# Optimization experiments

Hardware: AMD Instinct MI355X
Metric: run time of the kernel (lower is better)

The kernel has to match this reference:

```python
import jax, jax.numpy as jnp
import numpy as np

L, B, S, E, H, V = 2, 64, 64, 1024, 1024, 32000


def _uni(key, shape, k):
    return jax.random.uniform(key, shape, jnp.float32, -k, k)


def setup_inputs() -> dict:
    key = jax.random.key(0)
    ks = jax.random.split(key, 16)
    k = 1.0 / np.sqrt(H)
    inp = {
        "inputs": jax.random.randint(ks[0], (S, B), 0, V),
        "hidden": jnp.zeros((L, B, H), jnp.float32),
        "emb": jax.random.uniform(ks[1], (V, E), jnp.float32, -0.1, 0.1),
        # per-layer GRU weights stacked on leading L axis (layer0 input = emb = H)
        "Wx": _uni(ks[2], (L, H, H), k),   # linear_W (no bias), used for r gate
        "Ur": _uni(ks[3], (L, H, H), k),
        "br": _uni(ks[4], (L, H), k),
        "Wz": _uni(ks[5], (L, H, H), k),
        "Uz": _uni(ks[6], (L, H, H), k),
        "bz": _uni(ks[7], (L, H), k),
        "Wh": _uni(ks[8], (L, H, H), k),
        "Uh": _uni(ks[9], (L, H, H), k),
        "bh": _uni(ks[10], (L, H), k),
        "dec_W": jax.random.uniform(ks[11], (V, H), jnp.float32, -0.1, 0.1),
        "dec_b": jnp.zeros((V,), jnp.float32),
    }
    return inp


def _gru_cell(x, h, Wx, Ur, br, Wz, Uz, bz, Wh, Uh, bh):
    # faithful to GRU_Hidden.forward (r gate uses linear_W, bias-free W projections)
    r = jax.nn.sigmoid(x @ Wx.T + h @ Ur.T + br)
    z = jax.nn.sigmoid(x @ Wz.T + h @ Uz.T + bz)
    h_cand = jnp.tanh(x @ Wh.T + (r * h) @ Uh.T + bh)
    return (1.0 - z) * h + z * h_cand


def reference(inputs, hidden, emb, Wx, Ur, br, Wz, Uz, bz, Wh, Uh, bh, dec_W, dec_b):
    x_embs = emb[inputs]  # [S, B, E]; dropout is identity (dp_keep_prob = 1.0)
    n_layers = Wx.shape[0]

    def step(h, x_t):
        new_h = []
        inp = x_t
        for l in range(n_layers):
            hl = _gru_cell(inp, h[l], Wx[l], Ur[l], br[l], Wz[l], Uz[l], bz[l], Wh[l], Uh[l], bh[l])
            new_h.append(hl)
            inp = hl
        logits_t = inp @ dec_W.T + dec_b  # [B, V]
        return jnp.stack(new_h), logits_t

    h_final, logits = jax.lax.scan(step, hidden, x_embs)
    return logits, h_final
```

## Files before the change

kernel.cpp:

```cpp
#include <hip/hip_runtime.h>

#define SBV 131072000

typedef __bf16 bf16x8 __attribute__((ext_vector_type(8)));
typedef float  f32x4  __attribute__((ext_vector_type(4)));
typedef unsigned short u16;

__device__ __forceinline__ u16 f2bf(float f) {
  union { float f; unsigned u; } c; c.f = f;
  return (u16)((c.u + 0x7fffu + ((c.u >> 16) & 1u)) >> 16);
}
__device__ __forceinline__ float sigm(float x) { return 1.f / (1.f + __expf(-x)); }
__device__ __forceinline__ float tanh_f(float x) { return 2.f / (1.f + __expf(-2.f * x)) - 1.f; }


__global__ void k_cvtv(const float* __restrict__ src, u16* __restrict__ dst, int n4) {
  const float4* s4 = (const float4*)src;
  ushort4* d4 = (ushort4*)dst;
  for (int i = blockIdx.x * blockDim.x + threadIdx.x; i < n4; i += gridDim.x * blockDim.x) {
    float4 v = s4[i];
    ushort4 o; o.x = f2bf(v.x); o.y = f2bf(v.y); o.z = f2bf(v.z); o.w = f2bf(v.w);
    d4[i] = o;
  }
}

__global__ void k_pack3(const float* __restrict__ sx, const float* __restrict__ sz,
                        const float* __restrict__ sh, int srcOff, u16* __restrict__ dst) {
  int i = blockIdx.x * blockDim.x + threadIdx.x;
  if (i >= 786432) return;
  int g = i >> 18;
  int r4 = i & 262143;
  const float* s = (g == 0 ? sx : (g == 1 ? sz : sh)) + srcOff;
  float4 v = ((const float4*)s)[r4];
  ushort4 o; o.x = f2bf(v.x); o.y = f2bf(v.y); o.z = f2bf(v.z); o.w = f2bf(v.w);
  ((ushort4*)dst)[i] = o;
}

__global__ void k_embed(const int* __restrict__ idx, const float* __restrict__ emb,
                        u16* __restrict__ xe) {
  int i = blockIdx.x * blockDim.x + threadIdx.x;
  if (i >= 1048576) return;
  int row = i >> 8, k4 = i & 255;
  int e = idx[row];
  float4 v = ((const float4*)emb)[(size_t)e * 256 + k4];
  ushort4 o; o.x = f2bf(v.x); o.y = f2bf(v.y); o.z = f2bf(v.z); o.w = f2bf(v.w);
  ((ushort4*)xe)[i] = o;
}

__global__ __launch_bounds__(256) void gemm_bt(const u16* __restrict__ A, const u16* __restrict__ Bm,
                                               float* __restrict__ C, int M, int N, int K, int mtiles) {
  __shared__ u16 As[128 * 32];
  __shared__ u16 Bs[128 * 32];
  const int tid = threadIdx.x;
  const int bm = blockIdx.x % mtiles, bn = blockIdx.x / mtiles;
  const int m0 = bm * 128, n0 = bn * 128;
  const int lane = tid & 63, w = tid >> 6, wm = w & 1, wn = w >> 1;
  const int la = lane & 15, lk = lane >> 4;
  const int srow = tid >> 2, sk = (tid & 3) * 8;
  f32x4 acc[4][4] = {};
  for (int kt = 0; kt < K; kt += 32) {
    const u16* srcA0 = A + (size_t)(m0 + srow) * K + kt + sk;
    const u16* srcA1 = A + (size_t)(m0 + srow + 64) * K + kt + sk;
    const u16* srcB0 = Bm + (size_t)(n0 + srow) * K + kt + sk;
    const u16* srcB1 = Bm + (size_t)(n0 + srow + 64) * K + kt + sk;
    __builtin_amdgcn_global_load_lds((const __attribute__((address_space(1))) void*)srcA0,
        (__attribute__((address_space(3))) void*)((char*)As + tid * 16), 16, 0, 0);
    __builtin_amdgcn_global_load_lds((const __attribute__((address_space(1))) void*)srcA1,
        (__attribute__((address_space(3))) void*)((char*)As + 4096 + tid * 16), 16, 0, 0);
    __builtin_amdgcn_global_load_lds((const __attribute__((address_space(1))) void*)srcB0,
        (__attribute__((address_space(3))) void*)((char*)Bs + tid * 16), 16, 0, 0);
    __builtin_amdgcn_global_load_lds((const __attribute__((address_space(1))) void*)srcB1,
        (__attribute__((address_space(3))) void*)((char*)Bs + 4096 + tid * 16), 16, 0, 0);
    __syncthreads();
    bf16x8 av[4], bv[4];
    #pragma unroll
    for (int m = 0; m < 4; ++m)
      av[m] = *(const bf16x8*)(As + (wm * 64 + m * 16 + la) * 32 + lk * 8);
    #pragma unroll
    for (int n = 0; n < 4; ++n)
      bv[n] = *(const bf16x8*)(Bs + (wn * 64 + n * 16 + la) * 32 + lk * 8);
    #pragma unroll
    for (int m = 0; m < 4; ++m)
      #pragma unroll
      for (int n = 0; n < 4; ++n)
        acc[m][n] = __builtin_amdgcn_mfma_f32_16x16x32_bf16(av[m], bv[n], acc[m][n], 0, 0, 0);
    __syncthreads();
  }
  #pragma unroll
  for (int n = 0; n < 4; ++n) {
    const int gc = n0 + wn * 64 + n * 16 + la;
    #pragma unroll
    for (int m = 0; m < 4; ++m) {
      const int gr0 = m0 + wm * 64 + m * 16 + lk * 4;
      #pragma unroll
      for (int r = 0; r < 4; ++r)
        C[(size_t)(gr0 + r) * N + gc] = acc[m][n][r];
    }
  }
}


__device__ __forceinline__ void waitg64(const unsigned* f, unsigned tgt, int tid) {
  if (tgt && tid < 64) {
    unsigned g = 0;
    while (true) {
      bool ok = true;
      if (tid < 16) {
        uint4 v; const uint4* p = (const uint4*)f + tid;
        asm volatile("global_load_dwordx4 %0, %1, off sc1\ns_waitcnt vmcnt(0)"
                     : "=v"(v) : "v"(p) : "memory");
        ok = v.x >= tgt && v.y >= tgt && v.z >= tgt && v.w >= tgt;
      }
      if (__all(ok)) break;
      __builtin_amdgcn_s_sleep(1);
      if (++g > 1000000u) break;
    }
  }
  __syncthreads();
}

__device__ __forceinline__ void waitg2x(const unsigned* f0, unsigned t0,
                                        const unsigned* f1, unsigned t1, int tid) {
  if (tid < 64) {
    unsigned g = 0;
    while (true) {
      bool ok = true;
      if (tid < 32) {
        const unsigned* f = (tid < 16) ? f0 : f1;
        unsigned tgt = (tid < 16) ? t0 : t1;
        if (tgt) {
          uint4 v; const uint4* p = (const uint4*)f + (tid & 15);
          asm volatile("global_load_dwordx4 %0, %1, off sc1\ns_waitcnt vmcnt(0)"
                       : "=v"(v) : "v"(p) : "memory");
          ok = v.x >= tgt && v.y >= tgt && v.z >= tgt && v.w >= tgt;
        }
      }
      if (__all(ok)) break;
      __builtin_amdgcn_s_sleep(1);
      if (++g > 1000000u) break;
    }
  }
  __syncthreads();
}

__device__ __forceinline__ void arrive(unsigned* myFlag, unsigned val, int tid) {
  asm volatile("s_waitcnt vmcnt(0)" ::: "memory");
  __syncthreads();
  if (tid == 0)
    asm volatile("global_store_dword %0, %1, off sc1" :: "v"(myFlag), "v"(val) : "memory");
}

__global__ __launch_bounds__(256) void k_fused(
    const u16* __restrict__ hinitb,
    const float* __restrict__ hidden,
    const float* __restrict__ X0,
    const u16* __restrict__ Ucat0, const u16* __restrict__ Ucat1,
    const u16* __restrict__ Wcat1,
    const float* __restrict__ br, const float* __restrict__ bz, const float* __restrict__ bh,
    u16* __restrict__ H0seq, u16* __restrict__ H1seq,
    u16* __restrict__ RH0, u16* __restrict__ RH1,
    const u16* __restrict__ decWb,
    const float* __restrict__ decb,
    float* __restrict__ out,
    unsigned* flags) {
  extern __shared__ char sW[];
  const int tid = threadIdx.x, bid = blockIdx.x;
  const int lane = tid & 63, w = tid >> 6;
  const int la = lane & 15, lk = lane >> 4;

  __builtin_amdgcn_fence(__ATOMIC_ACQUIRE, "agent");

  if (bid >= 128) {
    const int d = bid - 128;
    const int c0 = d * 256 + w * 64;
    float bb[4];
    #pragma unroll
    for (int nf = 0; nf < 4; ++nf) bb[nf] = decb[c0 + nf * 16 + la];
    const u16* Bp[4];
    #pragma unroll
    for (int nf = 0; nf < 4; ++nf)
      Bp[nf] = decWb + (size_t)(c0 + nf * 16 + la) * 1024 + lk * 8;
    for (int t = 0; t < 64; ++t) {
      waitg64(flags + 64, 2 * t + 2, tid);
      const u16* Ab = H1seq + (size_t)t * 65536;
      const u16* Ap[4];
      #pragma unroll
      for (int mf = 0; mf < 4; ++mf) Ap[mf] = Ab + (mf * 16 + la) * 1024 + lk * 8;
      f32x4 acc[4][4] = {};
      #pragma unroll 4
      for (int ks = 0; ks < 32; ++ks) {
        bf16x8 av[4], bv[4];
        #pragma unroll
        for (int mf = 0; mf < 4; ++mf) av[mf] = *(const bf16x8*)(Ap[mf] + ks * 32);
        #pragma unroll
        for (int nf = 0; nf < 4; ++nf) bv[nf] = *(const bf16x8*)(Bp[nf] + ks * 32);
        #pragma unroll
        for (int mf = 0; mf < 4; ++mf)
          #pragma unroll
          for (int nf = 0; nf < 4; ++nf)
            acc[mf][nf] = __builtin_amdgcn_mfma_f32_16x16x32_bf16(av[mf], bv[nf], acc[mf][nf], 0, 0, 0);
      }
      #pragma unroll
      for (int mf = 0; mf < 4; ++mf)
        #pragma unroll
        for (int nf = 0; nf < 4; ++nf) {
          const size_t rb = (size_t)(t * 64 + mf * 16 + lk * 4) * 32000 + c0 + nf * 16 + la;
          #pragma unroll
          for (int r = 0; r < 4; ++r)
            out[rb + (size_t)r * 32000] = acc[mf][nf][r] + bb[nf];
        }
    }
    return;
  }

  const int layer = bid >> 6, jb = bid & 63, j0 = jb * 16;
  const int jl = j0 + la;
  const int row0 = w * 16;
  const u16* Ucat = layer ? Ucat1 : Ucat0;
  u16* Hseq = layer ? H1seq : H0seq;
  u16* RHl = layer ? RH1 : RH0;
  const u16* hinit = hinitb + layer * 65536;
  unsigned* fSelf = flags + layer * 64;
  const unsigned* fL0 = flags;
  unsigned* myFlag = fSelf + jb;
  float* houtf = out + (size_t)SBV;

  const int xorv = (la & 7) << 4;
  for (int i = 0; i < 24; ++i) {
    int c = i * 256 + tid;
    int g = c >> 11, rem = c & 2047;
    int urow = rem >> 7, kc = rem & 127;
    uint4 v = *(const uint4*)(Ucat + ((size_t)((g << 10) + j0 + urow)) * 1024 + kc * 8);
    *(uint4*)(sW + (g << 15) + urow * 2048 + ((kc * 16) ^ ((urow & 7) << 4))) = v;
  }
  __syncthreads();
  const char* sWla = sW + la * 2048;

  float h_reg[4], z_reg[4];
  #pragma unroll
  for (int r = 0; r < 4; ++r)
    h_reg[r] = hidden[layer * 65536 + (row0 + lk * 4 + r) * 1024 + jl];
  const float bR = br[layer * 1024 + jl], bZ = bz[layer * 1024 + jl], bH = bh[layer * 1024 + jl];

  const u16* WrR = Wcat1 + (size_t)(j0 + la) * 1024 + lk * 8;
  const u16* WrZ = WrR + (size_t)1024 * 1024;
  const u16* WrH = WrR + (size_t)2048 * 1024;

  for (int t = 0; t < 64; ++t) {
    if (layer == 0) waitg64(fSelf, 2 * t, tid);
    else            waitg2x(fSelf, 2 * t, fL0, 2 * t + 2, tid);
    const u16* hsrc = (t == 0) ? hinit : (Hseq + (size_t)(t - 1) * 65536);
    const u16* ap = hsrc + (size_t)(row0 + la) * 1024 + lk * 8;
    f32x4 accR = {0.f, 0.f, 0.f, 0.f}, accZ = {0.f, 0.f, 0.f, 0.f};
    if (layer == 0) {
      #pragma unroll 16
      for (int ks = 0; ks < 32; ++ks) {
        const int kx = (ks * 64 + lk * 16) ^ xorv;
        bf16x8 a = *(const bf16x8*)(ap + ks * 32);
        accR = __builtin_amdgcn_mfma_f32_16x16x32_bf16(a, *(const bf16x8*)(sWla + kx), accR, 0, 0, 0);
        accZ = __builtin_amdgcn_mfma_f32_16x16x32_bf16(a, *(const bf16x8*)(sWla + 32768 + kx), accZ, 0, 0, 0);
      }
    } else {
      const u16* xp = H0seq + (size_t)t * 65536 + (size_t)(row0 + la) * 1024 + lk * 8;
      #pragma unroll 8
      for (int ks = 0; ks < 32; ++ks) {
        const int kx = (ks * 64 + lk * 16) ^ xorv;
        bf16x8 a = *(const bf16x8*)(ap + ks * 32);
        bf16x8 x = *(const bf16x8*)(xp + ks * 32);
        accR = __builtin_amdgcn_mfma_f32_16x16x32_bf16(a, *(const bf16x8*)(sWla + kx), accR, 0, 0, 0);
        accZ = __builtin_amdgcn_mfma_f32_16x16x32_bf16(a, *(const bf16x8*)(sWla + 32768 + kx), accZ, 0, 0, 0);
        accR = __builtin_amdgcn_mfma_f32_16x16x32_bf16(x, *(const bf16x8*)(WrR + ks * 32), accR, 0, 0, 0);
        accZ = __builtin_amdgcn_mfma_f32_16x16x32_bf16(x, *(const bf16x8*)(WrZ + ks * 32), accZ, 0, 0, 0);
      }
    }
    #pragma unroll
    for (int r = 0; r < 4; ++r) {
      const int row = row0 + lk * 4 + r;
      float pr = accR[r] + bR, pz = accZ[r] + bZ;
      if (layer == 0) {
        const float* xf = X0 + (size_t)(t * 64 + row) * 3072 + jl;
        pr += xf[0]; pz += xf[1024];
      }
      float rv = sigm(pr);
      z_reg[r] = sigm(pz);
      unsigned v = f2bf(rv * h_reg[r]);
      u16* p = RHl + (size_t)(t * 64 + row) * 1024 + jl;
      asm volatile("global_store_short %0, %1, off sc1" :: "v"(p), "v"(v));
    }
    arrive(myFlag, 2 * t + 1, tid);
    waitg64(fSelf, 2 * t + 1, tid);
    const u16* rp = RHl + (size_t)t * 65536 + (size_t)(row0 + la) * 1024 + lk * 8;
    f32x4 accH = {0.f, 0.f, 0.f, 0.f};
    if (layer == 0) {
      #pragma unroll 16
      for (int ks = 0; ks < 32; ++ks) {
        const int kx = (ks * 64 + lk * 16) ^ xorv;
        bf16x8 a = *(const bf16x8*)(rp + ks * 32);
        accH = __builtin_amdgcn_mfma_f32_16x16x32_bf16(a, *(const bf16x8*)(sWla + 65536 + kx), accH, 0, 0, 0);
      }
    } else {
      const u16* xp = H0seq + (size_t)t * 65536 + (size_t)(row0 + la) * 1024 + lk * 8;
      #pragma unroll 8
      for (int ks = 0; ks < 32; ++ks) {
        const int kx = (ks * 64 + lk * 16) ^ xorv;
        bf16x8 a = *(const bf16x8*)(rp + ks * 32);
        bf16x8 x = *(const bf16x8*)(xp + ks * 32);
        accH = __builtin_amdgcn_mfma_f32_16x16x32_bf16(a, *(const bf16x8*)(sWla + 65536 + kx), accH, 0, 0, 0);
        accH = __builtin_amdgcn_mfma_f32_16x16x32_bf16(x, *(const bf16x8*)(WrH + ks * 32), accH, 0, 0, 0);
      }
    }
    #pragma unroll
    for (int r = 0; r < 4; ++r) {
      const int row = row0 + lk * 4 + r;
      float pre = accH[r] + bH;
      if (layer == 0) pre += X0[(size_t)(t * 64 + row) * 3072 + 2048 + jl];
      float hc = tanh_f(pre);
      float hn = h_reg[r] + z_reg[r] * (hc - h_reg[r]);
      h_reg[r] = hn;
      unsigned v = f2bf(hn);
      u16* p = Hseq + (size_t)(t * 64 + row) * 1024 + jl;
      asm volatile("global_store_short %0, %1, off sc1" :: "v"(p), "v"(v));
      if (t == 63) houtf[layer * 65536 + row * 1024 + jl] = hn;
    }
    arrive(myFlag, 2 * t + 2, tid);
  }
}

extern "C" void kernel_launch(void* const* d_in, const int* in_sizes, int n_in,
                              void* d_out, int out_size, void* d_ws, size_t ws_size,
                              hipStream_t stream) {
  const int* inputs = (const int*)d_in[0];
  const float* hidden = (const float*)d_in[1];
  const float* emb = (const float*)d_in[2];
  const float* Wx = (const float*)d_in[3];
  const float* Ur = (const float*)d_in[4];
  const float* br = (const float*)d_in[5];
  const float* Wz = (const float*)d_in[6];
  const float* Uz = (const float*)d_in[7];
  const float* bz = (const float*)d_in[8];
  const float* Wh = (const float*)d_in[9];
  const float* Uh = (const float*)d_in[10];
  const float* bh = (const float*)d_in[11];
  const float* decW = (const float*)d_in[12];
  const float* decb = (const float*)d_in[13];
  float* out = (float*)d_out;

  char* ws = (char*)d_ws;
  size_t off = 0;
  auto alloc = [&](size_t bytes) { char* p = ws + off; off += (bytes + 255) & ~(size_t)255; return p; };
  unsigned* flags = (unsigned*)alloc(4096);
  u16* hinitb = (u16*)alloc((size_t)2 * 64 * 1024 * 2);
  u16* xe     = (u16*)alloc((size_t)4096 * 1024 * 2);
  u16* Wcat0b = (u16*)alloc((size_t)3072 * 1024 * 2);
  u16* Wcat1b = (u16*)alloc((size_t)3072 * 1024 * 2);
  u16* Ucat0b = (u16*)alloc((size_t)3072 * 1024 * 2);
  u16* Ucat1b = (u16*)alloc((size_t)3072 * 1024 * 2);
  u16* decWb  = (u16*)alloc((size_t)32000 * 1024 * 2);
  float* X0   = (float*)alloc((size_t)4096 * 3072 * 4);
  u16* H0seq  = (u16*)alloc((size_t)4096 * 1024 * 2);
  u16* H1seq  = (u16*)alloc((size_t)4096 * 1024 * 2);
  u16* RH0    = (u16*)alloc((size_t)4096 * 1024 * 2);
  u16* RH1    = (u16*)alloc((size_t)4096 * 1024 * 2);

  hipMemsetAsync(flags, 0, 4096, stream);
  k_cvtv<<<128, 256, 0, stream>>>(hidden, hinitb, 32768);
  k_pack3<<<3072, 256, 0, stream>>>(Wx, Wz, Wh, 0, Wcat0b);
  k_pack3<<<3072, 256, 0, stream>>>(Wx, Wz, Wh, 1048576, Wcat1b);
  k_pack3<<<3072, 256, 0, stream>>>(Ur, Uz, Uh, 0, Ucat0b);
  k_pack3<<<3072, 256, 0, stream>>>(Ur, Uz, Uh, 1048576, Ucat1b);
  k_embed<<<4096, 256, 0, stream>>>(inputs, emb, xe);
  k_cvtv<<<4096, 256, 0, stream>>>(decW, decWb, 8192000);

  gemm_bt<<<768, 256, 0, stream>>>(xe, Wcat0b, X0, 4096, 3072, 1024, 32);

  (void)hipFuncSetAttribute(reinterpret_cast<const void*>(&k_fused),
                            hipFuncAttributeMaxDynamicSharedMemorySize, 98304);
  k_fused<<<253, 256, 98304, stream>>>(hinitb, hidden, X0, Ucat0b, Ucat1b, Wcat1b,
                                       br, bz, bh, H0seq, H1seq, RH0, RH1,
                                       decWb, decb, out, flags);
}
```

Before: 2.480 ms.

## Offload layer-1 input projection to dedicated blocks via ring buffer

Adds 16 helper blocks that compute the layer-1 input projection (H0 times Wcat1) for each timestep and write it into a ring of 8 fp32 slots reused from the xe workspace. They signal per-step flags, so layer-1 recurrent blocks only run the U-matrix MFMAs and read the precomputed x terms. The decoder is re-tiled into 100 blocks with 5 column fragments each. Spin-waits are changed to per-wave polling without block barriers and with shorter timeouts. This takes x-projection work off the serial recurrent critical path, at the cost of extra flag synchronization and ring-buffer global traffic.

Result: slower. 3.559 ms (+43.5%).

```diff
diff --git a/kernel.cpp b/kernel.cpp
--- a/kernel.cpp
+++ b/kernel.cpp
@@ -1,6 +1,10 @@
 #include <hip/hip_runtime.h>
 
-#define SBV 131072000
+#define SBV  131072000
+#define NRB  128
+#define NXW  16
+#define NDB  100
+#define RING 8
 
 typedef __bf16 bf16x8 __attribute__((ext_vector_type(8)));
 typedef float  f32x4  __attribute__((ext_vector_type(4)));
@@ -100,47 +104,57 @@
 }
 
 
-__device__ __forceinline__ void waitg64(const unsigned* f, unsigned tgt, int tid) {
-  if (tgt && tid < 64) {
-    unsigned g = 0;
-    while (true) {
-      bool ok = true;
-      if (tid < 16) {
-        uint4 v; const uint4* p = (const uint4*)f + tid;
+__device__ __forceinline__ void waitg64(const unsigned* f, unsigned tgt, int lane) {
+  if (!tgt) return;
+  unsigned g = 0;
+  while (true) {
+    bool ok = true;
+    if (lane < 16) {
+      uint4 v; const uint4* p = (const uint4*)f + lane;
+      asm volatile("global_load_dwordx4 %0, %1, off sc1\ns_waitcnt vmcnt(0)"
+                   : "=v"(v) : "v"(p) : "memory");
+      ok = v.x >= tgt && v.y >= tgt && v.z >= tgt && v.w >= tgt;
+    }
+    if (__all(ok)) break;
+    if (++g > 100000u) break;
+  }
+}
+
+__device__ __forceinline__ void waitg64s(const unsigned* f, unsigned tgt, int lane) {
+  unsigned g = 0;
+  while (true) {
+    bool ok = true;
+    if (lane < 16) {
+      uint4 v; const uint4* p = (const uint4*)f + lane;
+      asm volatile("global_load_dwordx4 %0, %1, off sc1\ns_waitcnt vmcnt(0)"
+                   : "=v"(v) : "v"(p) : "memory");
+      ok = v.x >= tgt && v.y >= tgt && v.z >= tgt && v.w >= tgt;
+    }
+    if (__all(ok)) break;
+    __builtin_amdgcn_s_sleep(1);
+    if (++g > 200000u) break;
+  }
+}
+
+__device__ __forceinline__ void waitL1A(const unsigned* fL1, unsigned t2,
+                                        const unsigned* fX1, unsigned tx, int lane) {
+  unsigned g = 0;
+  while (true) {
+    bool ok = true;
+    if (lane < 20) {
+      const uint4* p = (lane < 16) ? ((const uint4*)fL1 + lane)
+                                   : ((const uint4*)fX1 + (lane - 16));
+      const unsigned tgt = (lane < 16) ? t2 : tx;
+      if (tgt) {
+        uint4 v;
         asm volatile("global_load_dwordx4 %0, %1, off sc1\ns_waitcnt vmcnt(0)"
                      : "=v"(v) : "v"(p) : "memory");
         ok = v.x >= tgt && v.y >= tgt && v.z >= tgt && v.w >= tgt;
       }
-      if (__all(ok)) break;
-      __builtin_amdgcn_s_sleep(1);
-      if (++g > 1000000u) break;
-    }
-  }
-  __syncthreads();
-}
-
-__device__ __forceinline__ void waitg2x(const unsigned* f0, unsigned t0,
-                                        const unsigned* f1, unsigned t1, int tid) {
-  if (tid < 64) {
-    unsigned g = 0;
-    while (true) {
-      bool ok = true;
-      if (tid < 32) {
-        const unsigned* f = (tid < 16) ? f0 : f1;
-        unsigned tgt = (tid < 16) ? t0 : t1;
-        if (tgt) {
-          uint4 v; const uint4* p = (const uint4*)f + (tid & 15);
-          asm volatile("global_load_dwordx4 %0, %1, off sc1\ns_waitcnt vmcnt(0)"
-                       : "=v"(v) : "v"(p) : "memory");
-          ok = v.x >= tgt && v.y >= tgt && v.z >= tgt && v.w >= tgt;
-        }
-      }
-      if (__all(ok)) break;
-      __builtin_amdgcn_s_sleep(1);
-      if (++g > 1000000u) break;
-    }
-  }
-  __syncthreads();
+    }
+    if (__all(ok)) break;
+    if (++g > 100000u) break;
+  }
 }
 
 __device__ __forceinline__ void arrive(unsigned* myFlag, unsigned val, int tid) {
@@ -150,10 +164,12 @@
     asm volatile("global_store_dword %0, %1, off sc1" :: "v"(myFlag), "v"(val) : "memory");
 }
 
+
 __global__ __launch_bounds__(256) void k_fused(
     const u16* __restrict__ hinitb,
     const float* __restrict__ hidden,
     const float* __restrict__ X0,
+    float* __restrict__ ring,
     const u16* __restrict__ Ucat0, const u16* __restrict__ Ucat1,
     const u16* __restrict__ Wcat1,
     const float* __restrict__ br, const float* __restrict__ bz, const float* __restrict__ bh,
@@ -170,45 +186,77 @@
 
   __builtin_amdgcn_fence(__ATOMIC_ACQUIRE, "agent");
 
-  if (bid >= 128) {
-    const int d = bid - 128;
-    const int c0 = d * 256 + w * 64;
-    float bb[4];
-    #pragma unroll
-    for (int nf = 0; nf < 4; ++nf) bb[nf] = decb[c0 + nf * 16 + la];
-    const u16* Bp[4];
-    #pragma unroll
-    for (int nf = 0; nf < 4; ++nf)
+  unsigned* fL0 = flags;
+  unsigned* fL1 = flags + 64;
+  unsigned* fX1 = flags + 128;
+
+  if (bid >= NRB + NXW) {
+    const int d = bid - (NRB + NXW);
+    const int c0 = d * 320 + w * 80;
+    float bb[5];
+    const u16* Bp[5];
+    #pragma unroll
+    for (int nf = 0; nf < 5; ++nf) {
+      bb[nf] = decb[c0 + nf * 16 + la];
       Bp[nf] = decWb + (size_t)(c0 + nf * 16 + la) * 1024 + lk * 8;
+    }
     for (int t = 0; t < 64; ++t) {
-      waitg64(flags + 64, 2 * t + 2, tid);
+      waitg64s(fL1, 2 * t + 2, lane);
       const u16* Ab = H1seq + (size_t)t * 65536;
-      const u16* Ap[4];
-      #pragma unroll
-      for (int mf = 0; mf < 4; ++mf) Ap[mf] = Ab + (mf * 16 + la) * 1024 + lk * 8;
-      f32x4 acc[4][4] = {};
-      #pragma unroll 4
+      f32x4 acc[4][5] = {};
+      #pragma unroll 2
       for (int ks = 0; ks < 32; ++ks) {
-        bf16x8 av[4], bv[4];
-        #pragma unroll
-        for (int mf = 0; mf < 4; ++mf) av[mf] = *(const bf16x8*)(Ap[mf] + ks * 32);
-        #pragma unroll
-        for (int nf = 0; nf < 4; ++nf) bv[nf] = *(const bf16x8*)(Bp[nf] + ks * 32);
+        bf16x8 av[4], bv[5];
+        #pragma unroll
+        for (int mf = 0; mf < 4; ++mf)
+          av[mf] = *(const bf16x8*)(Ab + (mf * 16 + la) * 1024 + lk * 8 + ks * 32);
+        #pragma unroll
+        for (int nf = 0; nf < 5; ++nf) bv[nf] = *(const bf16x8*)(Bp[nf] + ks * 32);
         #pragma unroll
         for (int mf = 0; mf < 4; ++mf)
           #pragma unroll
-          for (int nf = 0; nf < 4; ++nf)
+          for (int nf = 0; nf < 5; ++nf)
             acc[mf][nf] = __builtin_amdgcn_mfma_f32_16x16x32_bf16(av[mf], bv[nf], acc[mf][nf], 0, 0, 0);
       }
       #pragma unroll
       for (int mf = 0; mf < 4; ++mf)
         #pragma unroll
-        for (int nf = 0; nf < 4; ++nf) {
+        for (int nf = 0; nf < 5; ++nf) {
           const size_t rb = (size_t)(t * 64 + mf * 16 + lk * 4) * 32000 + c0 + nf * 16 + la;
           #pragma unroll
           for (int r = 0; r < 4; ++r)
             out[rb + (size_t)r * 32000] = acc[mf][nf][r] + bb[nf];
         }
+    }
+    return;
+  }
+
+  if (bid >= NRB) {
+    const int idx = bid - NRB;
+    const int c0 = idx * 192;
+    const u16* Wb = Wcat1 + (size_t)(c0 + la) * 1024 + lk * 8;
+    unsigned* myFlag = fX1 + idx;
+    for (int t = 0; t < 64; ++t) {
+      waitg64(fL0, 2 * t + 2, lane);
+      if (t >= RING) waitg64(fL1, 2 * (t - RING) + 2, lane);
+      const u16* ap = H0seq + (size_t)t * 65536 + (w * 16 + la) * 1024 + lk * 8;
+      f32x4 acc[12] = {};
+      #pragma unroll 2
+      for (int ks = 0; ks < 32; ++ks) {
+        bf16x8 a = *(const bf16x8*)(ap + ks * 32);
+        #pragma unroll
+        for (int n = 0; n < 12; ++n)
+          acc[n] = __builtin_amdgcn_mfma_f32_16x16x32_bf16(a, *(const bf16x8*)(Wb + n * 16384 + ks * 32), acc[n], 0, 0, 0);
+      }
+      float* rbase = ring + (size_t)(t & (RING - 1)) * 196608 + (size_t)(w * 16 + lk * 4) * 3072 + c0 + la;
+      #pragma unroll
+      for (int n = 0; n < 12; ++n)
+        #pragma unroll
+        for (int r = 0; r < 4; ++r) {
+          float* p = rbase + (size_t)r * 3072 + n * 16;
+          asm volatile("global_store_dword %0, %1, off sc1" :: "v"(p), "v"(acc[n][r]) : "memory");
+        }
+      arrive(myFlag, t + 1, tid);
     }
     return;
   }
@@ -220,8 +268,7 @@
   u16* Hseq = layer ? H1seq : H0seq;
   u16* RHl = layer ? RH1 : RH0;
   const u16* hinit = hinitb + layer * 65536;
-  unsigned* fSelf = flags + layer * 64;
-  const unsigned* fL0 = flags;
+  unsigned* fSelf = layer ? fL1 : fL0;
   unsigned* myFlag = fSelf + jb;
   float* houtf = out + (size_t)SBV;
 
@@ -242,36 +289,31 @@
     h_reg[r] = hidden[layer * 65536 + (row0 + lk * 4 + r) * 1024 + jl];
   const float bR = br[layer * 1024 + jl], bZ = bz[layer * 1024 + jl], bH = bh[layer * 1024 + jl];
 
-  const u16* WrR = Wcat1 + (size_t)(j0 + la) * 1024 + lk * 8;
-  const u16* WrZ = WrR + (size_t)1024 * 1024;
-  const u16* WrH = WrR + (size_t)2048 * 1024;
-
   for (int t = 0; t < 64; ++t) {
-    if (layer == 0) waitg64(fSelf, 2 * t, tid);
-    else            waitg2x(fSelf, 2 * t, fL0, 2 * t + 2, tid);
+    float xr[4], xz[4];
+    if (layer == 0) {
+      waitg64(fL0, 2 * t, lane);
+    } else {
+      waitL1A(fL1, 2 * t, fX1, t + 1, lane);
+      const float* xb = ring + (size_t)(t & (RING - 1)) * 196608 + (size_t)(row0 + lk * 4) * 3072 + jl;
+      #pragma unroll
+      for (int r = 0; r < 4; ++r) {
+        const float* p0 = xb + (size_t)r * 3072;
+        const float* p1 = p0 + 1024;
+        asm volatile("global_load_dword %0, %1, off sc1" : "=v"(xr[r]) : "v"(p0) : "memory");
+        asm volatile("global_load_dword %0, %1, off sc1" : "=v"(xz[r]) : "v"(p1) : "memory");
+      }
+      asm volatile("s_waitcnt vmcnt(0)" ::: "memory");
+    }
     const u16* hsrc = (t == 0) ? hinit : (Hseq + (size_t)(t - 1) * 65536);
     const u16* ap = hsrc + (size_t)(row0 + la) * 1024 + lk * 8;
     f32x4 accR = {0.f, 0.f, 0.f, 0.f}, accZ = {0.f, 0.f, 0.f, 0.f};
-    if (layer == 0) {
-      #pragma unroll 16
-      for (int ks = 0; ks < 32; ++ks) {
-        const int kx = (ks * 64 + lk * 16) ^ xorv;
-        bf16x8 a = *(const bf16x8*)(ap + ks * 32);
-        accR = __builtin_amdgcn_mfma_f32_16x16x32_bf16(a, *(const bf16x8*)(sWla + kx), accR, 0, 0, 0);
-        accZ = __builtin_amdgcn_mfma_f32_16x16x32_bf16(a, *(const bf16x8*)(sWla + 32768 + kx), accZ, 0, 0, 0);
-      }
-    } else {
-      const u16* xp = H0seq + (size_t)t * 65536 + (size_t)(row0 + la) * 1024 + lk * 8;
-      #pragma unroll 8
-      for (int ks = 0; ks < 32; ++ks) {
-        const int kx = (ks * 64 + lk * 16) ^ xorv;
-        bf16x8 a = *(const bf16x8*)(ap + ks * 32);
-        bf16x8 x = *(const bf16x8*)(xp + ks * 32);
-        accR = __builtin_amdgcn_mfma_f32_16x16x32_bf16(a, *(const bf16x8*)(sWla + kx), accR, 0, 0, 0);
-        accZ = __builtin_amdgcn_mfma_f32_16x16x32_bf16(a, *(const bf16x8*)(sWla + 32768 + kx), accZ, 0, 0, 0);
-        accR = __builtin_amdgcn_mfma_f32_16x16x32_bf16(x, *(const bf16x8*)(WrR + ks * 32), accR, 0, 0, 0);
-        accZ = __builtin_amdgcn_mfma_f32_16x16x32_bf16(x, *(const bf16x8*)(WrZ + ks * 32), accZ, 0, 0, 0);
-      }
+    #pragma unroll 16
+    for (int ks = 0; ks < 32; ++ks) {
+      const int kx = (ks * 64 + lk * 16) ^ xorv;
+      bf16x8 a = *(const bf16x8*)(ap + ks * 32);
+      accR = __builtin_amdgcn_mfma_f32_16x16x32_bf16(a, *(const bf16x8*)(sWla + kx), accR, 0, 0, 0);
+      accZ = __builtin_amdgcn_mfma_f32_16x16x32_bf16(a, *(const bf16x8*)(sWla + 32768 + kx), accZ, 0, 0, 0);
     }
     #pragma unroll
     for (int r = 0; r < 4; ++r) {
@@ -280,6 +322,8 @@
       if (layer == 0) {
         const float* xf = X0 + (size_t)(t * 64 + row) * 3072 + jl;
         pr += xf[0]; pz += xf[1024];
+      } else {
+        pr += xr[r]; pz += xz[r];
       }
       float rv = sigm(pr);
       z_reg[r] = sigm(pz);
@@ -288,32 +332,31 @@
       asm volatile("global_store_short %0, %1, off sc1" :: "v"(p), "v"(v));
     }
     arrive(myFlag, 2 * t + 1, tid);
-    waitg64(fSelf, 2 * t + 1, tid);
+    waitg64(fSelf, 2 * t + 1, lane);
+    float xh[4];
+    if (layer == 1) {
+      const float* xb = ring + (size_t)(t & (RING - 1)) * 196608 + (size_t)(row0 + lk * 4) * 3072 + 2048 + jl;
+      #pragma unroll
+      for (int r = 0; r < 4; ++r) {
+        const float* p0 = xb + (size_t)r * 3072;
+        asm volatile("global_load_dword %0, %1, off sc1" : "=v"(xh[r]) : "v"(p0) : "memory");
+      }
+      asm volatile("s_waitcnt vmcnt(0)" ::: "memory");
+    }
     const u16* rp = RHl + (size_t)t * 65536 + (size_t)(row0 + la) * 1024 + lk * 8;
     f32x4 accH = {0.f, 0.f, 0.f, 0.f};
-    if (layer == 0) {
-      #pragma unroll 16
-      for (int ks = 0; ks < 32; ++ks) {
-        const int kx = (ks * 64 + lk * 16) ^ xorv;
-        bf16x8 a = *(const bf16x8*)(rp + ks * 32);
-        accH = __builtin_amdgcn_mfma_f32_16x16x32_bf16(a, *(const bf16x8*)(sWla + 65536 + kx), accH, 0, 0, 0);
-      }
-    } else {
-      const u16* xp = H0seq + (size_t)t * 65536 + (size_t)(row0 + la) * 1024 + lk * 8;
-      #pragma unroll 8
-      for (int ks = 0; ks < 32; ++ks) {
-        const int kx = (ks * 64 + lk * 16) ^ xorv;
-        bf16x8 a = *(const bf16x8*)(rp + ks * 32);
-        bf16x8 x = *(const bf16x8*)(xp + ks * 32);
-        accH = __builtin_amdgcn_mfma_f32_16x16x32_bf16(a, *(const bf16x8*)(sWla + 65536 + kx), accH, 0, 0, 0);
-        accH = __builtin_amdgcn_mfma_f32_16x16x32_bf16(x, *(const bf16x8*)(WrH + ks * 32), accH, 0, 0, 0);
-      }
+    #pragma unroll 16
+    for (int ks = 0; ks < 32; ++ks) {
+      const int kx = (ks * 64 + lk * 16) ^ xorv;
+      bf16x8 a = *(const bf16x8*)(rp + ks * 32);
+      accH = __builtin_amdgcn_mfma_f32_16x16x32_bf16(a, *(const bf16x8*)(sWla + 65536 + kx), accH, 0, 0, 0);
     }
     #pragma unroll
     for (int r = 0; r < 4; ++r) {
       const int row = row0 + lk * 4 + r;
       float pre = accH[r] + bH;
       if (layer == 0) pre += X0[(size_t)(t * 64 + row) * 3072 + 2048 + jl];
+      else            pre += xh[r];
       float hc = tanh_f(pre);
       float hn = h_reg[r] + z_reg[r] * (hc - h_reg[r]);
       h_reg[r] = hn;
@@ -361,6 +404,7 @@
   u16* H1seq  = (u16*)alloc((size_t)4096 * 1024 * 2);
   u16* RH0    = (u16*)alloc((size_t)4096 * 1024 * 2);
   u16* RH1    = (u16*)alloc((size_t)4096 * 1024 * 2);
+  float* ring = (float*)xe;
 
   hipMemsetAsync(flags, 0, 4096, stream);
   k_cvtv<<<128, 256, 0, stream>>>(hidden, hinitb, 32768);
@@ -375,7 +419,8 @@
 
   (void)hipFuncSetAttribute(reinterpret_cast<const void*>(&k_fused),
                             hipFuncAttributeMaxDynamicSharedMemorySize, 98304);
-  k_fused<<<253, 256, 98304, stream>>>(hinitb, hidden, X0, Ucat0b, Ucat1b, Wcat1b,
-                                       br, bz, bh, H0seq, H1seq, RH0, RH1,
-                                       decWb, decb, out, flags);
-}
+  k_fused<<<NRB + NXW + NDB, 256, 98304, stream>>>(hinitb, hidden, X0, ring,
+                                                   Ucat0b, Ucat1b, Wcat1b,
+                                                   br, bz, bh, H0seq, H1seq, RH0, RH1,
+                                                   decWb, decb, out, flags);
+}
```
